# Kernel tuning notes

Measured on AMD Instinct MI355X. Metric: run time of the kernel, lower is better.

Reference implementation:

```python
import jax, jax.numpy as jnp
import numpy as np

PAIR_CHANNELS = 128
N_HEADS = 8
MAX_PI_LENGTH = 8
NUM_IJKL = 1_000_000
NUM_IJK = 200_000
NUM_UIJK = 400_000
NUM_UIJKL = 3_000_000


def _segment_softmax(x, seg, num_seg):
    # numerically stable softmax within segments
    m = jax.ops.segment_max(x, seg, num_segments=num_seg)
    e = jnp.exp(x - m[seg])
    s = jax.ops.segment_sum(e, seg, num_segments=num_seg)
    return e / s[seg]


def setup_inputs() -> dict:
    key = jax.random.key(0)
    ks = jax.random.split(key, 10)
    d_cat = N_HEADS * (MAX_PI_LENGTH + 1)  # 72
    return {
        "prop_attr": jax.random.normal(ks[0], (NUM_UIJK, PAIR_CHANNELS), jnp.float32),
        "stereo_attr": jax.random.normal(ks[1], (NUM_IJKL, PAIR_CHANNELS), jnp.float32),
        "gather_idx_ijkl_jkl": jax.random.randint(ks[2], (NUM_IJKL,), 0, NUM_IJK),
        "gather_idx_Uijkl_ijkl": jax.random.randint(ks[3], (NUM_UIJKL,), 0, NUM_IJKL),
        "gather_idx_Uijkl_Uijk": jax.random.randint(ks[4], (NUM_UIJKL,), 0, NUM_UIJK),
        "gather_idx_Uijkl_ujkl": jax.random.randint(ks[5], (NUM_UIJKL,), 0, NUM_UIJK),
        "num_ijk": NUM_IJK,
        "num_Uijk": NUM_UIJK,
        "W_value": jax.random.normal(ks[6], (PAIR_CHANNELS, N_HEADS), jnp.float32) / np.float32(np.sqrt(PAIR_CHANNELS)),
        "W_kernel": jax.random.normal(ks[7], (PAIR_CHANNELS, N_HEADS), jnp.float32) / np.float32(np.sqrt(PAIR_CHANNELS)),
        "ln_scale": jnp.ones((d_cat,), jnp.float32),
        "ln_bias": jnp.zeros((d_cat,), jnp.float32),
        "W1": jax.random.normal(ks[8], (d_cat, d_cat), jnp.float32) / np.float32(np.sqrt(d_cat)),
        "b1": jnp.zeros((d_cat,), jnp.float32),
        "W2": jax.random.normal(ks[9], (d_cat, PAIR_CHANNELS), jnp.float32) / np.float32(np.sqrt(d_cat)),
        "b2": jnp.zeros((PAIR_CHANNELS,), jnp.float32),
    }


def reference(prop_attr, stereo_attr, gather_idx_ijkl_jkl, gather_idx_Uijkl_ijkl,
              gather_idx_Uijkl_Uijk, gather_idx_Uijkl_ujkl, num_ijk, num_Uijk,
              W_value, W_kernel, ln_scale, ln_bias, W1, b1, W2, b2):
    # attention-like kernel over triangle pairs, normalized within jkl segments
    kernel_logits = stereo_attr @ W_kernel                       # [num_ijkl, H]
    alpha = _segment_softmax(kernel_logits, gather_idx_ijkl_jkl, num_ijk)
    kernel = alpha[gather_idx_Uijkl_ijkl]                        # [num_Uijkl, H]

    # iterative gather -> mul -> segment_sum propagation
    outs = [prop_attr @ W_value]                                 # [num_Uijk, H]
    for _ in range(MAX_PI_LENGTH):
        g = outs[-1][gather_idx_Uijkl_Uijk]                      # [num_Uijkl, H]
        outs.append(jax.ops.segment_sum(kernel * g, gather_idx_Uijkl_ujkl,
                                        num_segments=num_Uijk))
    x = jnp.concatenate(outs, axis=-1)                           # [num_Uijk, H*(L+1)]

    # GELUMLP: LayerNorm -> Linear -> GELU(exact) -> Linear
    mu = jnp.mean(x, axis=-1, keepdims=True)
    var = jnp.var(x, axis=-1, keepdims=True)
    x = (x - mu) * jax.lax.rsqrt(var + 1e-5) * ln_scale + ln_bias
    x = jax.nn.gelu(x @ W1 + b1, approximate=False)
    x = x @ W2 + b2
    return x + prop_attr
```

## Files before the change

kernel.cpp:

```cpp
#include <hip/hip_runtime.h>
#include <math.h>

#define CH 128
#define NH 8
#define DCAT 72
#define NIJK 200000
#define SCAN_BLK 1024

typedef float f4 __attribute__((ext_vector_type(4)));
typedef float f2 __attribute__((ext_vector_type(2)));
typedef unsigned int u2 __attribute__((ext_vector_type(2)));
typedef unsigned int u4 __attribute__((ext_vector_type(4)));

static __device__ __forceinline__ f4 ntload4(const float* p) {
  return __builtin_nontemporal_load((const f4*)p);
}
static __device__ __forceinline__ f4 ld4(const float* p) {
  return *(const f4*)p;
}
static __device__ __forceinline__ void st4(float* p, f4 v) {
  *(f4*)p = v;
}
static __device__ __forceinline__ unsigned pack_bf16x2(float lo, float hi) {
  unsigned ul = __float_as_uint(lo);
  unsigned uh = __float_as_uint(hi);
  ul += 0x7FFFu + ((ul >> 16) & 1u);
  uh += 0x7FFFu + ((uh >> 16) & 1u);
  return (ul >> 16) | (uh & 0xFFFF0000u);
}
static __device__ __forceinline__ float bf_lo(unsigned u) {
  return __uint_as_float(u << 16);
}
static __device__ __forceinline__ float bf_hi(unsigned u) {
  return __uint_as_float(u & 0xFFFF0000u);
}

__global__ __launch_bounds__(256, 4) void k_logits(
    const float* __restrict__ stereo, const int* __restrict__ seg,
    const float* __restrict__ Wk, float* __restrict__ alpha,
    float* __restrict__ denom, int n) {
  __shared__ __align__(16) float sWt[NH][132];
  __shared__ __align__(16) float sS[64][132];
  int t = threadIdx.x;
  for (int i = t; i < NH * CH; i += 256) {
    int h = i >> 7, c = i & 127;
    sWt[h][c] = Wk[c * NH + h];
  }
  int base = blockIdx.x * 64;
  for (int i = t; i < 64 * 32; i += 256) {
    int row = i >> 5, c4 = i & 31;
    int rc = base + row < n ? base + row : n - 1;
    st4(&sS[row][c4 * 4], ntload4(stereo + (size_t)rc * CH + c4 * 4));
  }
  __syncthreads();
  int rr = t >> 3, h = t & 7;
  int r0 = base + rr, r1 = base + rr + 32;
  const float* wt = &sWt[h][0];
  float acc0 = 0.f, acc1 = 0.f;
#pragma unroll 4
  for (int c4 = 0; c4 < 32; ++c4) {
    f4 w = ld4(wt + c4 * 4);
    f4 a = ld4(&sS[rr][c4 * 4]);
    f4 b = ld4(&sS[rr + 32][c4 * 4]);
    acc0 = fmaf(a.w, w.w, fmaf(a.z, w.z, fmaf(a.y, w.y, fmaf(a.x, w.x, acc0))));
    acc1 = fmaf(b.w, w.w, fmaf(b.z, w.z, fmaf(b.y, w.y, fmaf(b.x, w.x, acc1))));
  }
  if (r0 < n) {
    float e = expf(acc0);
    alpha[(size_t)r0 * NH + h] = e;
    unsafeAtomicAdd(&denom[(size_t)seg[r0] * NH + h], e);
  }
  if (r1 < n) {
    float e = expf(acc1);
    alpha[(size_t)r1 * NH + h] = e;
    unsafeAtomicAdd(&denom[(size_t)seg[r1] * NH + h], e);
  }
}

__global__ __launch_bounds__(256) void k_norm(
    const float* __restrict__ alpha, const float* __restrict__ denom,
    const int* __restrict__ seg, unsigned* __restrict__ alpha2, int n) {
  int idx = (blockIdx.x * 256 + threadIdx.x) * 4;
  if (idx < n * NH) {
    int r = idx >> 3;
    f4 a = ld4(alpha + idx);
    f4 d = ld4(denom + (size_t)seg[r] * NH + (idx & 7));
    u2 o;
    o.x = pack_bf16x2(a.x / d.x, a.y / d.y);
    o.y = pack_bf16x2(a.z / d.z, a.w / d.w);
    *(u2*)(alpha2 + (idx >> 1)) = o;
  }
}

__global__ __launch_bounds__(256, 4) void k_value(
    const float* __restrict__ prop, const float* __restrict__ Wv,
    unsigned* __restrict__ x0, int n) {
  __shared__ __align__(16) float sWt[NH][132];
  __shared__ __align__(16) float sS[64][132];
  int t = threadIdx.x;
  for (int i = t; i < NH * CH; i += 256) {
    int h = i >> 7, c = i & 127;
    sWt[h][c] = Wv[c * NH + h];
  }
  int base = blockIdx.x * 64;
  for (int i = t; i < 64 * 32; i += 256) {
    int row = i >> 5, c4 = i & 31;
    int rc = base + row < n ? base + row : n - 1;
    st4(&sS[row][c4 * 4], ntload4(prop + (size_t)rc * CH + c4 * 4));
  }
  __syncthreads();
  int rr = t >> 3, h = t & 7;
  int r0 = base + rr, r1 = base + rr + 32;
  const float* wt = &sWt[h][0];
  float acc0 = 0.f, acc1 = 0.f;
#pragma unroll 4
  for (int c4 = 0; c4 < 32; ++c4) {
    f4 w = ld4(wt + c4 * 4);
    f4 a = ld4(&sS[rr][c4 * 4]);
    f4 b = ld4(&sS[rr + 32][c4 * 4]);
    acc0 = fmaf(a.w, w.w, fmaf(a.z, w.z, fmaf(a.y, w.y, fmaf(a.x, w.x, acc0))));
    acc1 = fmaf(b.w, w.w, fmaf(b.z, w.z, fmaf(b.y, w.y, fmaf(b.x, w.x, acc1))));
  }
  float p0 = __shfl_xor(acc0, 1);
  float p1 = __shfl_xor(acc1, 1);
  if ((h & 1) == 0) {
    if (r0 < n) x0[(size_t)r0 * 4 + (h >> 1)] = pack_bf16x2(acc0, p0);
    if (r1 < n) x0[(size_t)r1 * 4 + (h >> 1)] = pack_bf16x2(acc1, p1);
  }
}

__global__ __launch_bounds__(256) void k_hist(
    const int* __restrict__ g5, int* __restrict__ counts, int n) {
  int i = blockIdx.x * 256 + threadIdx.x;
  if (i < n) atomicAdd(&counts[g5[i]], 1);
}

__global__ __launch_bounds__(256) void k_scan1(
    const int* __restrict__ counts, int* __restrict__ excl,
    int* __restrict__ bsum, int n) {
  __shared__ int s[256];
  int b = blockIdx.x, t = threadIdx.x;
  int base = b * SCAN_BLK + t * 4;
  int v0 = base + 0 < n ? counts[base + 0] : 0;
  int v1 = base + 1 < n ? counts[base + 1] : 0;
  int v2 = base + 2 < n ? counts[base + 2] : 0;
  int v3 = base + 3 < n ? counts[base + 3] : 0;
  int p0 = v0, p1 = p0 + v1, p2 = p1 + v2, sum = p2 + v3;
  s[t] = sum;
  __syncthreads();
  for (int d = 1; d < 256; d <<= 1) {
    int tv = (t >= d) ? s[t - d] : 0;
    __syncthreads();
    s[t] += tv;
    __syncthreads();
  }
  int texcl = s[t] - sum;
  if (t == 255) bsum[b] = s[255];
  if (base + 0 < n) excl[base + 0] = texcl;
  if (base + 1 < n) excl[base + 1] = texcl + p0;
  if (base + 2 < n) excl[base + 2] = texcl + p1;
  if (base + 3 < n) excl[base + 3] = texcl + p2;
}

__global__ __launch_bounds__(256) void k_scan2(int* __restrict__ bsum, int nb) {
  __shared__ int s[512];
  int t = threadIdx.x;
  for (int i = t; i < nb; i += 256) s[i] = bsum[i];
  __syncthreads();
  if (t == 0) {
    int run = 0;
    for (int i = 0; i < nb; ++i) { int c = s[i]; s[i] = run; run += c; }
    s[nb] = run;
  }
  __syncthreads();
  for (int i = t; i <= nb; i += 256) bsum[i] = s[i];
}

__global__ __launch_bounds__(256) void k_scan3(
    int* __restrict__ rowstart, int* __restrict__ cursor,
    const int* __restrict__ bsum, int n, int nb) {
  int i = blockIdx.x * 256 + threadIdx.x;
  if (i < n) {
    int r = rowstart[i] + bsum[i >> 10];
    rowstart[i] = r;
    cursor[i] = r;
  }
  if (i == 0) rowstart[n] = bsum[nb];
}

__global__ __launch_bounds__(256) void k_scatter(
    const int* __restrict__ g3, const int* __restrict__ g4,
    const int* __restrict__ g5, int* __restrict__ cursor,
    const unsigned* __restrict__ alpha2,
    int* __restrict__ sI4, unsigned* __restrict__ salpha, int n) {
  int i = blockIdx.x * 256 + threadIdx.x;
  if (i >= n) return;
  int pos = atomicAdd(&cursor[g5[i]], 1);
  sI4[pos] = g4[i];
  u4 a = *(const u4*)(alpha2 + (size_t)g3[i] * 4);
  *(u4*)(salpha + (size_t)pos * 4) = a;
}

#define FMA8(A0, A1, AV, GV) \
  A0.x = fmaf(bf_lo(AV.x), bf_lo(GV.x), A0.x); \
  A0.y = fmaf(bf_hi(AV.x), bf_hi(GV.x), A0.y); \
  A0.z = fmaf(bf_lo(AV.y), bf_lo(GV.y), A0.z); \
  A0.w = fmaf(bf_hi(AV.y), bf_hi(GV.y), A0.w); \
  A1.x = fmaf(bf_lo(AV.z), bf_lo(GV.z), A1.x); \
  A1.y = fmaf(bf_hi(AV.z), bf_hi(GV.z), A1.y); \
  A1.z = fmaf(bf_lo(AV.w), bf_lo(GV.w), A1.z); \
  A1.w = fmaf(bf_hi(AV.w), bf_hi(GV.w), A1.w);

__global__ __launch_bounds__(256) void k_spmv(
    const unsigned* __restrict__ salpha, const int* __restrict__ rowstart,
    const int* __restrict__ sI4, const unsigned* __restrict__ xsrc,
    unsigned* __restrict__ xdst, int n) {
  int p = blockIdx.x * 256 + threadIdx.x;
  if (p >= n) return;
  int s = rowstart[p], e = rowstart[p + 1];
  f4 accA = {0.f, 0.f, 0.f, 0.f};
  f4 accB = {0.f, 0.f, 0.f, 0.f};
  int k = s;
  for (; k + 4 <= e; k += 4) {
    int i0 = __builtin_nontemporal_load(sI4 + k + 0);
    int i1 = __builtin_nontemporal_load(sI4 + k + 1);
    int i2v = __builtin_nontemporal_load(sI4 + k + 2);
    int i3 = __builtin_nontemporal_load(sI4 + k + 3);
    u4 a0 = __builtin_nontemporal_load((const u4*)(salpha + (size_t)(k + 0) * 4));
    u4 a1 = __builtin_nontemporal_load((const u4*)(salpha + (size_t)(k + 1) * 4));
    u4 a2 = __builtin_nontemporal_load((const u4*)(salpha + (size_t)(k + 2) * 4));
    u4 a3 = __builtin_nontemporal_load((const u4*)(salpha + (size_t)(k + 3) * 4));
    u4 g0 = *(const u4*)(xsrc + (size_t)i0 * 4);
    u4 g1 = *(const u4*)(xsrc + (size_t)i1 * 4);
    u4 g2 = *(const u4*)(xsrc + (size_t)i2v * 4);
    u4 g3v = *(const u4*)(xsrc + (size_t)i3 * 4);
    FMA8(accA, accB, a0, g0)
    FMA8(accA, accB, a1, g1)
    FMA8(accA, accB, a2, g2)
    FMA8(accA, accB, a3, g3v)
  }
  for (; k < e; ++k) {
    int i0 = sI4[k];
    u4 a0 = __builtin_nontemporal_load((const u4*)(salpha + (size_t)k * 4));
    u4 g0 = *(const u4*)(xsrc + (size_t)i0 * 4);
    FMA8(accA, accB, a0, g0)
  }
  u4 o;
  o.x = pack_bf16x2(accA.x, accA.y);
  o.y = pack_bf16x2(accA.z, accA.w);
  o.z = pack_bf16x2(accB.x, accB.y);
  o.w = pack_bf16x2(accB.z, accB.w);
  *(u4*)(xdst + (size_t)p * 4) = o;
}
#undef FMA8

__global__ __launch_bounds__(256) void k_mlp(
    const unsigned* __restrict__ xs, const float* __restrict__ prop,
    const float* __restrict__ lns, const float* __restrict__ lnb,
    const float* __restrict__ W1, const float* __restrict__ b1,
    const float* __restrict__ W2, const float* __restrict__ b2,
    float* __restrict__ out, int n) {
  __shared__ __align__(16) float sW1[DCAT][DCAT];
  __shared__ __align__(16) float sW2[DCAT][CH];
  __shared__ __align__(16) float sb1[DCAT];
  __shared__ __align__(16) float sb2[CH];
  __shared__ __align__(16) float slns[DCAT];
  __shared__ __align__(16) float slnb[DCAT];
  __shared__ __align__(16) float sx[64][DCAT];
  int t = threadIdx.x;
  for (int i = t; i < DCAT * DCAT; i += 256) sW1[0][i] = W1[i];
  for (int i = t; i < DCAT * CH; i += 256) sW2[0][i] = W2[i];
  if (t < DCAT) { sb1[t] = b1[t]; slns[t] = lns[t]; slnb[t] = lnb[t]; }
  if (t < CH) sb2[t] = b2[t];
  __syncthreads();
  int r = t >> 3, jg = t & 7;
  const int cs = 64 + jg;
  for (int base = blockIdx.x * 64; base < n; base += gridDim.x * 64) {
    int rows = min(64, n - base);
#pragma unroll
    for (int t2 = 0; t2 < 9; ++t2) {
      const unsigned* src = xs + (size_t)t2 * n * 4 + (size_t)base * 4;
      for (int i = t; i < rows * 4; i += 256) {
        unsigned v = src[i];
        int row = i >> 2, c2 = (i & 3) * 2;
        sx[row][t2 * NH + c2] = bf_lo(v);
        sx[row][t2 * NH + c2 + 1] = bf_hi(v);
      }
    }
    __syncthreads();
    int ra = r, rb = r + 32;
    bool va = ra < rows, vb = rb < rows;
    f2 xpA[4], xpB[4];
    float sumA = 0.f, sqA = 0.f, sumB = 0.f, sqB = 0.f;
#pragma unroll
    for (int m = 0; m < 4; ++m) {
      xpA[m] = *(const f2*)&sx[ra][2 * jg + 16 * m];
      xpB[m] = *(const f2*)&sx[rb][2 * jg + 16 * m];
      sumA += xpA[m].x + xpA[m].y; sqA += xpA[m].x * xpA[m].x + xpA[m].y * xpA[m].y;
      sumB += xpB[m].x + xpB[m].y; sqB += xpB[m].x * xpB[m].x + xpB[m].y * xpB[m].y;
    }
    float xsa = sx[ra][cs], xsb = sx[rb][cs];
    sumA += xsa; sqA += xsa * xsa;
    sumB += xsb; sqB += xsb * xsb;
    sumA += __shfl_xor(sumA, 1); sumA += __shfl_xor(sumA, 2); sumA += __shfl_xor(sumA, 4);
    sqA  += __shfl_xor(sqA, 1);  sqA  += __shfl_xor(sqA, 2);  sqA  += __shfl_xor(sqA, 4);
    sumB += __shfl_xor(sumB, 1); sumB += __shfl_xor(sumB, 2); sumB += __shfl_xor(sumB, 4);
    sqB  += __shfl_xor(sqB, 1);  sqB  += __shfl_xor(sqB, 2);  sqB  += __shfl_xor(sqB, 4);
    float muA = sumA * (1.f / 72.f);
    float rstdA = rsqrtf(sqA * (1.f / 72.f) - muA * muA + 1e-5f);
    float muB = sumB * (1.f / 72.f);
    float rstdB = rsqrtf(sqB * (1.f / 72.f) - muB * muB + 1e-5f);
#pragma unroll
    for (int m = 0; m < 4; ++m) {
      int cc = 2 * jg + 16 * m;
      f2 s = *(const f2*)&slns[cc];
      f2 o = *(const f2*)&slnb[cc];
      f2 w;
      w.x = (xpA[m].x - muA) * rstdA * s.x + o.x;
      w.y = (xpA[m].y - muA) * rstdA * s.y + o.y;
      *(f2*)&sx[ra][cc] = w;
      w.x = (xpB[m].x - muB) * rstdB * s.x + o.x;
      w.y = (xpB[m].y - muB) * rstdB * s.y + o.y;
      *(f2*)&sx[rb][cc] = w;
    }
    sx[ra][cs] = (xsa - muA) * rstdA * slns[cs] + slnb[cs];
    sx[rb][cs] = (xsb - muB) * rstdB * slns[cs] + slnb[cs];
    float accA[9], accB[9];
#pragma unroll
    for (int m = 0; m < 4; ++m) {
      f2 b = *(const f2*)&sb1[2 * jg + 16 * m];
      accA[2 * m] = b.x; accA[2 * m + 1] = b.y;
      accB[2 * m] = b.x; accB[2 * m + 1] = b.y;
    }
    accA[8] = sb1[cs]; accB[8] = accA[8];
    for (int k = 0; k < DCAT; k += 2) {
      f2 xa = *(const f2*)&sx[ra][k];
      f2 xb = *(const f2*)&sx[rb][k];
#pragma unroll
      for (int kk = 0; kk < 2; ++kk) {
        float xav = kk ? xa.y : xa.x;
        float xbv = kk ? xb.y : xb.x;
#pragma unroll
        for (int m = 0; m < 4; ++m) {
          f2 w = *(const f2*)&sW1[k + kk][2 * jg + 16 * m];
          accA[2 * m]     = fmaf(xav, w.x, accA[2 * m]);
          accA[2 * m + 1] = fmaf(xav, w.y, accA[2 * m + 1]);
          accB[2 * m]     = fmaf(xbv, w.x, accB[2 * m]);
          accB[2 * m + 1] = fmaf(xbv, w.y, accB[2 * m + 1]);
        }
        float ws = sW1[k + kk][cs];
        accA[8] = fmaf(xav, ws, accA[8]);
        accB[8] = fmaf(xbv, ws, accB[8]);
      }
    }
#define GELU(v) (0.5f * (v) * (1.f + erff((v) * 0.70710678118654752f)))
#pragma unroll
    for (int m = 0; m < 4; ++m) {
      int cc = 2 * jg + 16 * m;
      f2 g;
      g.x = GELU(accA[2 * m]); g.y = GELU(accA[2 * m + 1]);
      *(f2*)&sx[ra][cc] = g;
      g.x = GELU(accB[2 * m]); g.y = GELU(accB[2 * m + 1]);
      *(f2*)&sx[rb][cc] = g;
    }
    sx[ra][cs] = GELU(accA[8]);
    sx[rb][cs] = GELU(accB[8]);
    float acc2A[16], acc2B[16];
#pragma unroll
    for (int m = 0; m < 8; ++m) {
      f2 b = *(const f2*)&sb2[2 * jg + 16 * m];
      acc2A[2 * m] = b.x; acc2A[2 * m + 1] = b.y;
      acc2B[2 * m] = b.x; acc2B[2 * m + 1] = b.y;
    }
    for (int j = 0; j < DCAT; j += 2) {
      f2 ha = *(const f2*)&sx[ra][j];
      f2 hb = *(const f2*)&sx[rb][j];
#pragma unroll
      for (int jj = 0; jj < 2; ++jj) {
        float hav = jj ? ha.y : ha.x;
        float hbv = jj ? hb.y : hb.x;
#pragma unroll
        for (int m = 0; m < 8; ++m) {
          f2 w = *(const f2*)&sW2[j + jj][2 * jg + 16 * m];
          acc2A[2 * m]     = fmaf(hav, w.x, acc2A[2 * m]);
          acc2A[2 * m + 1] = fmaf(hav, w.y, acc2A[2 * m + 1]);
          acc2B[2 * m]     = fmaf(hbv, w.x, acc2B[2 * m]);
          acc2B[2 * m + 1] = fmaf(hbv, w.y, acc2B[2 * m + 1]);
        }
      }
    }
    if (va) {
      size_t ob = (size_t)(base + ra) * CH;
#pragma unroll
      for (int m = 0; m < 8; ++m) {
        int cc = 2 * jg + 16 * m;
        f2 pv = *(const f2*)(prop + ob + cc);
        f2 o;
        o.x = acc2A[2 * m] + pv.x;
        o.y = acc2A[2 * m + 1] + pv.y;
        *(f2*)(out + ob + cc) = o;
      }
    }
    if (vb) {
      size_t ob = (size_t)(base + rb) * CH;
#pragma unroll
      for (int m = 0; m < 8; ++m) {
        int cc = 2 * jg + 16 * m;
        f2 pv = *(const f2*)(prop + ob + cc);
        f2 o;
        o.x = acc2B[2 * m] + pv.x;
        o.y = acc2B[2 * m + 1] + pv.y;
        *(f2*)(out + ob + cc) = o;
      }
    }
    __syncthreads();
  }
}

extern "C" void kernel_launch(void* const* d_in, const int* in_sizes, int n_in,
                              void* d_out, int out_size, void* d_ws, size_t ws_size,
                              hipStream_t stream) {
  const float* prop   = (const float*)d_in[0];
  const float* stereo = (const float*)d_in[1];
  const int* g_jkl    = (const int*)d_in[2];
  const int* g3       = (const int*)d_in[3];
  const int* g4       = (const int*)d_in[4];
  const int* g5       = (const int*)d_in[5];
  const float* Wv     = (const float*)d_in[8];
  const float* Wk     = (const float*)d_in[9];
  const float* lns    = (const float*)d_in[10];
  const float* lnb    = (const float*)d_in[11];
  const float* W1     = (const float*)d_in[12];
  const float* b1     = (const float*)d_in[13];
  const float* W2     = (const float*)d_in[14];
  const float* b2     = (const float*)d_in[15];

  const int n_ijkl  = in_sizes[1] / CH;
  const int n_uijk  = in_sizes[0] / CH;
  const int n_uijkl = in_sizes[3];
  const int n_ijk   = NIJK;

  const int nb_scan = (n_uijk + SCAN_BLK - 1) / SCAN_BLK;

  auto al = [](size_t v) { return (v + 3) & ~(size_t)3; };
  size_t rs_off   = 0;
  size_t si4_off  = al(rs_off + (size_t)n_uijk + 1);
  size_t sal_off  = al(si4_off + (size_t)n_uijkl);
  size_t xs_off   = al(sal_off + (size_t)n_uijkl * 4);
  size_t a2_off   = al(xs_off + (size_t)n_uijk * 36);
  size_t a_off    = xs_off;
  size_t dn_off   = al(a_off + (size_t)n_ijkl * NH);
  size_t cnt_off  = al(dn_off + (size_t)n_ijk * NH);
  size_t cur_off  = al(cnt_off + (size_t)n_uijk);
  size_t bs_off   = al(cur_off + (size_t)n_uijk);

  float* base     = (float*)d_ws;
  int*   rowstart = (int*)(base + rs_off);
  int*   sI4      = (int*)(base + si4_off);
  unsigned* salpha= (unsigned*)(base + sal_off);
  unsigned* xs    = (unsigned*)(base + xs_off);
  unsigned* alpha2= (unsigned*)(base + a2_off);
  float* alpha    = base + a_off;
  float* denom    = base + dn_off;
  int*   counts   = (int*)(base + cnt_off);
  int*   cursor   = (int*)(base + cur_off);
  int*   bsum     = (int*)(base + bs_off);

  (void)hipMemsetAsync(denom, 0, (cur_off - dn_off) * sizeof(float), stream);

  k_hist<<<(n_uijkl + 255) / 256, 256, 0, stream>>>(g5, counts, n_uijkl);
  k_scan1<<<nb_scan, 256, 0, stream>>>(counts, rowstart, bsum, n_uijk);
  k_scan2<<<1, 256, 0, stream>>>(bsum, nb_scan);
  k_scan3<<<(n_uijk + 255) / 256, 256, 0, stream>>>(rowstart, cursor, bsum, n_uijk, nb_scan);

  k_logits<<<(n_ijkl + 63) / 64, 256, 0, stream>>>(stereo, g_jkl, Wk, alpha, denom, n_ijkl);
  k_norm<<<(n_ijkl * NH / 4 + 255) / 256, 256, 0, stream>>>(alpha, denom, g_jkl, alpha2, n_ijkl);
  k_scatter<<<(n_uijkl + 255) / 256, 256, 0, stream>>>(g3, g4, g5, cursor, alpha2, sI4, salpha, n_uijkl);

  k_value<<<(n_uijk + 63) / 64, 256, 0, stream>>>(prop, Wv, xs, n_uijk);
  for (int t = 0; t < 8; ++t) {
    const unsigned* xsrc = xs + (size_t)t * n_uijk * 4;
    unsigned* xdst = xs + (size_t)(t + 1) * n_uijk * 4;
    k_spmv<<<(n_uijk + 255) / 256, 256, 0, stream>>>(salpha, rowstart, sI4, xsrc, xdst, n_uijk);
  }
  k_mlp<<<512, 256, 0, stream>>>(xs, prop, lns, lnb, W1, b1, W2, b2, (float*)d_out, n_uijk);
}
```

Before: 1.390 ms.

## Split head dimension into two halves for SpMV propagation passes

Splits the 8-head bf16 state and the alpha weights into two 4-head planes, then runs the eight SpMV propagation steps separately for each half. Each gather now fetches 8 bytes instead of 16, which shrinks the random-access working set of each pass so it fits better in cache. The cost is twice as many SpMV launches and reading the index and rowstart arrays twice.

```diff
diff --git a/kernel.cpp b/kernel.cpp
--- a/kernel.cpp
+++ b/kernel.cpp
@@ -94,7 +94,7 @@
 
 __global__ __launch_bounds__(256, 4) void k_value(
     const float* __restrict__ prop, const float* __restrict__ Wv,
-    unsigned* __restrict__ x0, int n) {
+    unsigned* __restrict__ x0A, unsigned* __restrict__ x0B, int n) {
   __shared__ __align__(16) float sWt[NH][132];
   __shared__ __align__(16) float sS[64][132];
   int t = threadIdx.x;
@@ -124,8 +124,10 @@
   float p0 = __shfl_xor(acc0, 1);
   float p1 = __shfl_xor(acc1, 1);
   if ((h & 1) == 0) {
-    if (r0 < n) x0[(size_t)r0 * 4 + (h >> 1)] = pack_bf16x2(acc0, p0);
-    if (r1 < n) x0[(size_t)r1 * 4 + (h >> 1)] = pack_bf16x2(acc1, p1);
+    unsigned* dst = h < 4 ? x0A : x0B;
+    int w = (h >> 1) & 1;
+    if (r0 < n) dst[(size_t)r0 * 2 + w] = pack_bf16x2(acc0, p0);
+    if (r1 < n) dst[(size_t)r1 * 2 + w] = pack_bf16x2(acc1, p1);
   }
 }
 
@@ -192,24 +194,25 @@
     const int* __restrict__ g3, const int* __restrict__ g4,
     const int* __restrict__ g5, int* __restrict__ cursor,
     const unsigned* __restrict__ alpha2,
-    int* __restrict__ sI4, unsigned* __restrict__ salpha, int n) {
+    int* __restrict__ sI4, unsigned* __restrict__ salA,
+    unsigned* __restrict__ salB, int n) {
   int i = blockIdx.x * 256 + threadIdx.x;
   if (i >= n) return;
   int pos = atomicAdd(&cursor[g5[i]], 1);
   sI4[pos] = g4[i];
   u4 a = *(const u4*)(alpha2 + (size_t)g3[i] * 4);
-  *(u4*)(salpha + (size_t)pos * 4) = a;
-}
-
-#define FMA8(A0, A1, AV, GV) \
-  A0.x = fmaf(bf_lo(AV.x), bf_lo(GV.x), A0.x); \
-  A0.y = fmaf(bf_hi(AV.x), bf_hi(GV.x), A0.y); \
-  A0.z = fmaf(bf_lo(AV.y), bf_lo(GV.y), A0.z); \
-  A0.w = fmaf(bf_hi(AV.y), bf_hi(GV.y), A0.w); \
-  A1.x = fmaf(bf_lo(AV.z), bf_lo(GV.z), A1.x); \
-  A1.y = fmaf(bf_hi(AV.z), bf_hi(GV.z), A1.y); \
-  A1.z = fmaf(bf_lo(AV.w), bf_lo(GV.w), A1.z); \
-  A1.w = fmaf(bf_hi(AV.w), bf_hi(GV.w), A1.w);
+  u2 lo, hi;
+  lo.x = a.x; lo.y = a.y;
+  hi.x = a.z; hi.y = a.w;
+  *(u2*)(salA + (size_t)pos * 2) = lo;
+  *(u2*)(salB + (size_t)pos * 2) = hi;
+}
+
+#define FMA4H(ACC, AV, GV) \
+  ACC.x = fmaf(bf_lo(AV.x), bf_lo(GV.x), ACC.x); \
+  ACC.y = fmaf(bf_hi(AV.x), bf_hi(GV.x), ACC.y); \
+  ACC.z = fmaf(bf_lo(AV.y), bf_lo(GV.y), ACC.z); \
+  ACC.w = fmaf(bf_hi(AV.y), bf_hi(GV.y), ACC.w);
 
 __global__ __launch_bounds__(256) void k_spmv(
     const unsigned* __restrict__ salpha, const int* __restrict__ rowstart,
@@ -218,44 +221,42 @@
   int p = blockIdx.x * 256 + threadIdx.x;
   if (p >= n) return;
   int s = rowstart[p], e = rowstart[p + 1];
-  f4 accA = {0.f, 0.f, 0.f, 0.f};
-  f4 accB = {0.f, 0.f, 0.f, 0.f};
+  f4 acc = {0.f, 0.f, 0.f, 0.f};
   int k = s;
   for (; k + 4 <= e; k += 4) {
     int i0 = __builtin_nontemporal_load(sI4 + k + 0);
     int i1 = __builtin_nontemporal_load(sI4 + k + 1);
     int i2v = __builtin_nontemporal_load(sI4 + k + 2);
     int i3 = __builtin_nontemporal_load(sI4 + k + 3);
-    u4 a0 = __builtin_nontemporal_load((const u4*)(salpha + (size_t)(k + 0) * 4));
-    u4 a1 = __builtin_nontemporal_load((const u4*)(salpha + (size_t)(k + 1) * 4));
-    u4 a2 = __builtin_nontemporal_load((const u4*)(salpha + (size_t)(k + 2) * 4));
-    u4 a3 = __builtin_nontemporal_load((const u4*)(salpha + (size_t)(k + 3) * 4));
-    u4 g0 = *(const u4*)(xsrc + (size_t)i0 * 4);
-    u4 g1 = *(const u4*)(xsrc + (size_t)i1 * 4);
-    u4 g2 = *(const u4*)(xsrc + (size_t)i2v * 4);
-    u4 g3v = *(const u4*)(xsrc + (size_t)i3 * 4);
-    FMA8(accA, accB, a0, g0)
-    FMA8(accA, accB, a1, g1)
-    FMA8(accA, accB, a2, g2)
-    FMA8(accA, accB, a3, g3v)
+    u2 a0 = __builtin_nontemporal_load((const u2*)(salpha + (size_t)(k + 0) * 2));
+    u2 a1 = __builtin_nontemporal_load((const u2*)(salpha + (size_t)(k + 1) * 2));
+    u2 a2 = __builtin_nontemporal_load((const u2*)(salpha + (size_t)(k + 2) * 2));
+    u2 a3 = __builtin_nontemporal_load((const u2*)(salpha + (size_t)(k + 3) * 2));
+    u2 g0 = *(const u2*)(xsrc + (size_t)i0 * 2);
+    u2 g1 = *(const u2*)(xsrc + (size_t)i1 * 2);
+    u2 g2 = *(const u2*)(xsrc + (size_t)i2v * 2);
+    u2 g3v = *(const u2*)(xsrc + (size_t)i3 * 2);
+    FMA4H(acc, a0, g0)
+    FMA4H(acc, a1, g1)
+    FMA4H(acc, a2, g2)
+    FMA4H(acc, a3, g3v)
   }
   for (; k < e; ++k) {
     int i0 = sI4[k];
-    u4 a0 = __builtin_nontemporal_load((const u4*)(salpha + (size_t)k * 4));
-    u4 g0 = *(const u4*)(xsrc + (size_t)i0 * 4);
-    FMA8(accA, accB, a0, g0)
-  }
-  u4 o;
-  o.x = pack_bf16x2(accA.x, accA.y);
-  o.y = pack_bf16x2(accA.z, accA.w);
-  o.z = pack_bf16x2(accB.x, accB.y);
-  o.w = pack_bf16x2(accB.z, accB.w);
-  *(u4*)(xdst + (size_t)p * 4) = o;
-}
-#undef FMA8
+    u2 a0 = __builtin_nontemporal_load((const u2*)(salpha + (size_t)k * 2));
+    u2 g0 = *(const u2*)(xsrc + (size_t)i0 * 2);
+    FMA4H(acc, a0, g0)
+  }
+  u2 o;
+  o.x = pack_bf16x2(acc.x, acc.y);
+  o.y = pack_bf16x2(acc.z, acc.w);
+  *(u2*)(xdst + (size_t)p * 2) = o;
+}
+#undef FMA4H
 
 __global__ __launch_bounds__(256) void k_mlp(
-    const unsigned* __restrict__ xs, const float* __restrict__ prop,
+    const unsigned* __restrict__ xsA, const unsigned* __restrict__ xsB,
+    const float* __restrict__ prop,
     const float* __restrict__ lns, const float* __restrict__ lnb,
     const float* __restrict__ W1, const float* __restrict__ b1,
     const float* __restrict__ W2, const float* __restrict__ b2,
@@ -279,10 +280,12 @@
     int rows = min(64, n - base);
 #pragma unroll
     for (int t2 = 0; t2 < 9; ++t2) {
-      const unsigned* src = xs + (size_t)t2 * n * 4 + (size_t)base * 4;
       for (int i = t; i < rows * 4; i += 256) {
-        unsigned v = src[i];
-        int row = i >> 2, c2 = (i & 3) * 2;
+        int row = i >> 2, q = i & 3;
+        const unsigned* src = (q < 2 ? xsA : xsB) + (size_t)t2 * n * 2
+                              + (size_t)(base + row) * 2 + (q & 1);
+        unsigned v = *src;
+        int c2 = q * 2;
         sx[row][t2 * NH + c2] = bf_lo(v);
         sx[row][t2 * NH + c2 + 1] = bf_hi(v);
       }
@@ -445,10 +448,12 @@
   auto al = [](size_t v) { return (v + 3) & ~(size_t)3; };
   size_t rs_off   = 0;
   size_t si4_off  = al(rs_off + (size_t)n_uijk + 1);
-  size_t sal_off  = al(si4_off + (size_t)n_uijkl);
-  size_t xs_off   = al(sal_off + (size_t)n_uijkl * 4);
-  size_t a2_off   = al(xs_off + (size_t)n_uijk * 36);
-  size_t a_off    = xs_off;
+  size_t salA_off = al(si4_off + (size_t)n_uijkl);
+  size_t salB_off = al(salA_off + (size_t)n_uijkl * 2);
+  size_t xsA_off  = al(salB_off + (size_t)n_uijkl * 2);
+  size_t xsB_off  = al(xsA_off + (size_t)n_uijk * 18);
+  size_t a2_off   = al(xsB_off + (size_t)n_uijk * 18);
+  size_t a_off    = xsA_off;
   size_t dn_off   = al(a_off + (size_t)n_ijkl * NH);
   size_t cnt_off  = al(dn_off + (size_t)n_ijk * NH);
   size_t cur_off  = al(cnt_off + (size_t)n_uijk);
@@ -457,8 +462,10 @@
   float* base     = (float*)d_ws;
   int*   rowstart = (int*)(base + rs_off);
   int*   sI4      = (int*)(base + si4_off);
-  unsigned* salpha= (unsigned*)(base + sal_off);
-  unsigned* xs    = (unsigned*)(base + xs_off);
+  unsigned* salA  = (unsigned*)(base + salA_off);
+  unsigned* salB  = (unsigned*)(base + salB_off);
+  unsigned* xsA   = (unsigned*)(base + xsA_off);
+  unsigned* xsB   = (unsigned*)(base + xsB_off);
   unsigned* alpha2= (unsigned*)(base + a2_off);
   float* alpha    = base + a_off;
   float* denom    = base + dn_off;
@@ -475,13 +482,17 @@
 
   k_logits<<<(n_ijkl + 63) / 64, 256, 0, stream>>>(stereo, g_jkl, Wk, alpha, denom, n_ijkl);
   k_norm<<<(n_ijkl * NH / 4 + 255) / 256, 256, 0, stream>>>(alpha, denom, g_jkl, alpha2, n_ijkl);
-  k_scatter<<<(n_uijkl + 255) / 256, 256, 0, stream>>>(g3, g4, g5, cursor, alpha2, sI4, salpha, n_uijkl);
-
-  k_value<<<(n_uijk + 63) / 64, 256, 0, stream>>>(prop, Wv, xs, n_uijk);
-  for (int t = 0; t < 8; ++t) {
-    const unsigned* xsrc = xs + (size_t)t * n_uijk * 4;
-    unsigned* xdst = xs + (size_t)(t + 1) * n_uijk * 4;
-    k_spmv<<<(n_uijk + 255) / 256, 256, 0, stream>>>(salpha, rowstart, sI4, xsrc, xdst, n_uijk);
-  }
-  k_mlp<<<512, 256, 0, stream>>>(xs, prop, lns, lnb, W1, b1, W2, b2, (float*)d_out, n_uijk);
-}
+  k_scatter<<<(n_uijkl + 255) / 256, 256, 0, stream>>>(g3, g4, g5, cursor, alpha2, sI4, salA, salB, n_uijkl);
+
+  k_value<<<(n_uijk + 63) / 64, 256, 0, stream>>>(prop, Wv, xsA, xsB, n_uijk);
+  for (int half = 0; half < 2; ++half) {
+    unsigned* xh = half ? xsB : xsA;
+    unsigned* sal = half ? salB : salA;
+    for (int t = 0; t < 8; ++t) {
+      const unsigned* xsrc = xh + (size_t)t * n_uijk * 2;
+      unsigned* xdst = xh + (size_t)(t + 1) * n_uijk * 2;
+      k_spmv<<<(n_uijk + 255) / 256, 256, 0, stream>>>(sal, rowstart, sI4, xsrc, xdst, n_uijk);
+    }
+  }
+  k_mlp<<<512, 256, 0, stream>>>(xsA, xsB, prop, lns, lnb, W1, b1, W2, b2, (float*)d_out, n_uijk);
+}
```

After: 1.666 ms. 19.9% more time.
